# Kernel tuning notes

Measured on AMD Instinct MI355X. Metric: run time of the kernel, lower is better.

Reference implementation:

```python
import jax, jax.numpy as jnp
import numpy as np


def _edt_sq(binary):
    """Exact squared Euclidean distance transform of a 2D array.

    Nonzero pixels = foreground, zero pixels = background (scipy
    distance_transform_edt semantics). Computed as two separable 1D
    min-plus passes: d(i) = min_j (i-j)^2 + f(j), which is exact for EDT.
    """
    H, W = binary.shape
    INF = jnp.float32(H * H + W * W + 1)  # larger than any real sq distance
    f = jnp.where(binary == 0, jnp.float32(0.0), INF)  # [H, W]

    ih = jnp.arange(H, dtype=jnp.float32)
    sqh = (ih[:, None] - ih[None, :]) ** 2  # [H, H]
    # pass along rows (axis 0): d1[i, w] = min_j sqh[i, j] + f[j, w]
    d1 = jnp.min(sqh[:, :, None] + f[None, :, :], axis=1)  # [H, W]

    iw = jnp.arange(W, dtype=jnp.float32)
    sqw = (iw[:, None] - iw[None, :]) ** 2  # [W, W]
    # pass along cols (axis 1): d2[h, k] = min_l sqw[k, l] + d1[h, l]
    d2 = jnp.min(d1[:, None, :] + sqw[None, :, :], axis=2)  # [H, W]
    return d2


def setup_inputs() -> dict:
    key = jax.random.key(0)
    masks = jax.random.randint(key, (512, 512), 0, 2).astype(jnp.float32)
    return {"masks": masks}


def reference(masks):
    masks_n = masks / jnp.max(masks)          # masks / np.max(masks)
    dis_map = jnp.sqrt(_edt_sq(masks_n))      # distance_transform_edt
    skeleton = dis_map / jnp.max(dis_map)     # normalize
    boundary = masks_n - skeleton
    return (skeleton, boundary)
```

## Files before the change

kernel.cpp:

```cpp
#include <hip/hip_runtime.h>

#define H 512
#define W 512
#define N (H * W)
#define INF_SQ 524289.0f
#define KA_BLOCKS 1024
#define KB_BLOCKS 512

__global__ __launch_bounds__(256)
void edt2d_k(const float* __restrict__ masks, float* __restrict__ dis,
             float* __restrict__ pmaxm, float* __restrict__ pmaxd) {
    const int idx = blockIdx.x * 256 + threadIdx.x;
    const int y = idx >> 9, x = idx & (W - 1);

    const float v = masks[idx];
    float best = (v == 0.0f) ? 0.0f : INF_SQ;

    for (int r = 1; (float)(r * r) < best; ++r) {
        const int rr = r * r;
        const int ym = y - r, yp = y + r;
        const int x0 = max(x - r, 0), x1 = min(x + r, W - 1);
        if (ym >= 0) {
            const float* row = masks + ym * W;
            for (int x2 = x0; x2 <= x1; ++x2)
                if (row[x2] == 0.0f) {
                    const int dx = x2 - x;
                    best = fminf(best, (float)(dx * dx + rr));
                }
        }
        if (yp < H) {
            const float* row = masks + yp * W;
            for (int x2 = x0; x2 <= x1; ++x2)
                if (row[x2] == 0.0f) {
                    const int dx = x2 - x;
                    best = fminf(best, (float)(dx * dx + rr));
                }
        }
        const int y0 = max(y - r + 1, 0), y1 = min(y + r - 1, H - 1);
        if (x - r >= 0) {
            for (int y2 = y0; y2 <= y1; ++y2)
                if (masks[y2 * W + x - r] == 0.0f) {
                    const int dy = y2 - y;
                    best = fminf(best, (float)(dy * dy + rr));
                }
        }
        if (x + r < W) {
            for (int y2 = y0; y2 <= y1; ++y2)
                if (masks[y2 * W + x + r] == 0.0f) {
                    const int dy = y2 - y;
                    best = fminf(best, (float)(dy * dy + rr));
                }
        }
    }

    const float d = sqrtf(best);
    dis[idx] = d;

    float mm = v, md = d;
    for (int off = 32; off > 0; off >>= 1) {
        mm = fmaxf(mm, __shfl_down(mm, off, 64));
        md = fmaxf(md, __shfl_down(md, off, 64));
    }
    __shared__ float sm[4], sd[4];
    const int w = threadIdx.x >> 6, lane = threadIdx.x & 63;
    if (lane == 0) { sm[w] = mm; sd[w] = md; }
    __syncthreads();
    if (threadIdx.x == 0) {
        for (int i = 1; i < 4; ++i) { mm = fmaxf(mm, sm[i]); md = fmaxf(md, sd[i]); }
        pmaxm[blockIdx.x] = mm;
        pmaxd[blockIdx.x] = md;
    }
}

__global__ __launch_bounds__(128)
void finalize_k(const float* __restrict__ masks,
                const float* __restrict__ pmaxm,
                const float* __restrict__ pmaxd,
                float* __restrict__ out) {
    const int t = threadIdx.x;

    float mm = 0.0f, md = 0.0f;
#pragma unroll
    for (int i = 0; i < KA_BLOCKS / 128; ++i) {
        mm = fmaxf(mm, pmaxm[t + i * 128]);
        md = fmaxf(md, pmaxd[t + i * 128]);
    }
    for (int off = 32; off > 0; off >>= 1) {
        mm = fmaxf(mm, __shfl_down(mm, off, 64));
        md = fmaxf(md, __shfl_down(md, off, 64));
    }
    __shared__ float sm[2], sd[2];
    if ((t & 63) == 0) { sm[t >> 6] = mm; sd[t >> 6] = md; }
    __syncthreads();
    const float maxm = fmaxf(sm[0], sm[1]);
    const float maxd = fmaxf(sd[0], sd[1]);

    const int i = blockIdx.x * 128 + t;
    const float4 d4 = ((const float4*)out)[i];
    const float4 m4 = ((const float4*)masks)[i];
    float4 sk, bd;
    sk.x = d4.x / maxd; sk.y = d4.y / maxd; sk.z = d4.z / maxd; sk.w = d4.w / maxd;
    bd.x = m4.x / maxm - sk.x; bd.y = m4.y / maxm - sk.y;
    bd.z = m4.z / maxm - sk.z; bd.w = m4.w / maxm - sk.w;
    ((float4*)out)[i] = sk;
    ((float4*)out)[N / 4 + i] = bd;
}

extern "C" void kernel_launch(void* const* d_in, const int* in_sizes, int n_in,
                              void* d_out, int out_size, void* d_ws, size_t ws_size,
                              hipStream_t stream) {
    const float* masks = (const float*)d_in[0];
    float* out = (float*)d_out;
    float* pmaxm = (float*)d_ws;
    float* pmaxd = pmaxm + KA_BLOCKS;

    hipLaunchKernelGGL(edt2d_k, dim3(KA_BLOCKS), dim3(256), 0, stream, masks, out, pmaxm, pmaxd);
    hipLaunchKernelGGL(finalize_k, dim3(KB_BLOCKS), dim3(128), 0, stream, masks, pmaxm, pmaxd, out);
}
```

Baseline: 13.43 us.

## Process four pixels per thread with vectorized 3x3 neighborhood precheck

Each thread now handles four horizontally adjacent pixels, loading the three surrounding rows as float4 plus edge scalars and resolving the radius-1 ring from registers. Only pixels whose nearest background lies beyond distance one fall back to the ring-search loop, starting at radius 2. The EDT kernel's block count drops fourfold, and the finalize reduction reads fewer partial maxima. The change removes scattered scalar global loads for the common case but lowers thread-level parallelism and adds serialization when one of a thread's four pixels needs the slow path.

```diff
diff --git a/kernel.cpp b/kernel.cpp
--- a/kernel.cpp
+++ b/kernel.cpp
@@ -4,59 +4,105 @@
 #define W 512
 #define N (H * W)
 #define INF_SQ 524289.0f
-#define KA_BLOCKS 1024
+#define KA_BLOCKS 256
 #define KB_BLOCKS 512
 
 __global__ __launch_bounds__(256)
 void edt2d_k(const float* __restrict__ masks, float* __restrict__ dis,
              float* __restrict__ pmaxm, float* __restrict__ pmaxd) {
-    const int idx = blockIdx.x * 256 + threadIdx.x;
-    const int y = idx >> 9, x = idx & (W - 1);
+    const int tid = blockIdx.x * 256 + threadIdx.x;
+    const int y = tid >> 7;
+    const int q = tid & 127;
+    const int x0 = q << 2;
 
-    const float v = masks[idx];
-    float best = (v == 0.0f) ? 0.0f : INF_SQ;
+    const float4* m4 = (const float4*)masks;
+    const int yu = (y > 0) ? y - 1 : 0;
+    const int yd = (y < H - 1) ? y + 1 : H - 1;
 
-    for (int r = 1; (float)(r * r) < best; ++r) {
-        const int rr = r * r;
-        const int ym = y - r, yp = y + r;
-        const int x0 = max(x - r, 0), x1 = min(x + r, W - 1);
-        if (ym >= 0) {
-            const float* row = masks + ym * W;
-            for (int x2 = x0; x2 <= x1; ++x2)
-                if (row[x2] == 0.0f) {
-                    const int dx = x2 - x;
-                    best = fminf(best, (float)(dx * dx + rr));
-                }
-        }
-        if (yp < H) {
-            const float* row = masks + yp * W;
-            for (int x2 = x0; x2 <= x1; ++x2)
-                if (row[x2] == 0.0f) {
-                    const int dx = x2 - x;
-                    best = fminf(best, (float)(dx * dx + rr));
-                }
-        }
-        const int y0 = max(y - r + 1, 0), y1 = min(y + r - 1, H - 1);
-        if (x - r >= 0) {
-            for (int y2 = y0; y2 <= y1; ++y2)
-                if (masks[y2 * W + x - r] == 0.0f) {
-                    const int dy = y2 - y;
-                    best = fminf(best, (float)(dy * dy + rr));
-                }
-        }
-        if (x + r < W) {
-            for (int y2 = y0; y2 <= y1; ++y2)
-                if (masks[y2 * W + x + r] == 0.0f) {
-                    const int dy = y2 - y;
-                    best = fminf(best, (float)(dy * dy + rr));
-                }
-        }
+    const float4 u4 = m4[(yu << 7) + q];
+    const float4 c4 = m4[(y << 7) + q];
+    const float4 d4 = m4[(yd << 7) + q];
+
+    const int xl = (x0 > 0) ? x0 - 1 : 0;
+    const int xr = (x0 + 4 < W) ? x0 + 4 : W - 1;
+    const float ul = masks[yu * W + xl], ur = masks[yu * W + xr];
+    const float cl = masks[y * W + xl],  cr = masks[y * W + xr];
+    const float dl = masks[yd * W + xl], dr = masks[yd * W + xr];
+
+    const bool vy0 = (y > 0), vy1 = (y < H - 1);
+    const bool vx0 = (x0 > 0), vx1 = (x0 + 4 < W);
+
+    const float rowU[6] = {ul, u4.x, u4.y, u4.z, u4.w, ur};
+    const float rowC[6] = {cl, c4.x, c4.y, c4.z, c4.w, cr};
+    const float rowD[6] = {dl, d4.x, d4.y, d4.z, d4.w, dr};
+
+    float best[4];
+#pragma unroll
+    for (int j = 0; j < 4; ++j) {
+        const bool lv = (j > 0) || vx0;
+        const bool rv = (j < 3) || vx1;
+        float b = INF_SQ;
+        b = fminf(b, (vy0 && lv && rowU[j] == 0.0f)     ? 2.0f : INF_SQ);
+        b = fminf(b, (vy0 &&       rowU[j + 1] == 0.0f) ? 1.0f : INF_SQ);
+        b = fminf(b, (vy0 && rv && rowU[j + 2] == 0.0f) ? 2.0f : INF_SQ);
+        b = fminf(b, (lv &&        rowC[j] == 0.0f)     ? 1.0f : INF_SQ);
+        b = fminf(b, (rv &&        rowC[j + 2] == 0.0f) ? 1.0f : INF_SQ);
+        b = fminf(b, (vy1 && lv && rowD[j] == 0.0f)     ? 2.0f : INF_SQ);
+        b = fminf(b, (vy1 &&       rowD[j + 1] == 0.0f) ? 1.0f : INF_SQ);
+        b = fminf(b, (vy1 && rv && rowD[j + 2] == 0.0f) ? 2.0f : INF_SQ);
+        best[j] = (rowC[j + 1] == 0.0f) ? 0.0f : b;
     }
 
-    const float d = sqrtf(best);
-    dis[idx] = d;
+#pragma unroll
+    for (int j = 0; j < 4; ++j) {
+        const int x = x0 + j;
+        float b = best[j];
+        for (int r = 2; (float)(r * r) < b; ++r) {
+            const int rr = r * r;
+            const int ymr = y - r, ypr = y + r;
+            const int xa = max(x - r, 0), xb = min(x + r, W - 1);
+            if (ymr >= 0) {
+                const float* row = masks + ymr * W;
+                for (int x2 = xa; x2 <= xb; ++x2)
+                    if (row[x2] == 0.0f) {
+                        const int dx = x2 - x;
+                        b = fminf(b, (float)(dx * dx + rr));
+                    }
+            }
+            if (ypr < H) {
+                const float* row = masks + ypr * W;
+                for (int x2 = xa; x2 <= xb; ++x2)
+                    if (row[x2] == 0.0f) {
+                        const int dx = x2 - x;
+                        b = fminf(b, (float)(dx * dx + rr));
+                    }
+            }
+            const int y0 = max(y - r + 1, 0), y1 = min(y + r - 1, H - 1);
+            if (x - r >= 0) {
+                for (int y2 = y0; y2 <= y1; ++y2)
+                    if (masks[y2 * W + x - r] == 0.0f) {
+                        const int dy = y2 - y;
+                        b = fminf(b, (float)(dy * dy + rr));
+                    }
+            }
+            if (x + r < W) {
+                for (int y2 = y0; y2 <= y1; ++y2)
+                    if (masks[y2 * W + x + r] == 0.0f) {
+                        const int dy = y2 - y;
+                        b = fminf(b, (float)(dy * dy + rr));
+                    }
+            }
+        }
+        best[j] = b;
+    }
 
-    float mm = v, md = d;
+    float4 o;
+    o.x = sqrtf(best[0]); o.y = sqrtf(best[1]);
+    o.z = sqrtf(best[2]); o.w = sqrtf(best[3]);
+    ((float4*)dis)[tid] = o;
+
+    float mm = fmaxf(fmaxf(c4.x, c4.y), fmaxf(c4.z, c4.w));
+    float md = fmaxf(fmaxf(o.x, o.y), fmaxf(o.z, o.w));
     for (int off = 32; off > 0; off >>= 1) {
         mm = fmaxf(mm, __shfl_down(mm, off, 64));
         md = fmaxf(md, __shfl_down(md, off, 64));
@@ -79,12 +125,8 @@
                 float* __restrict__ out) {
     const int t = threadIdx.x;
 
-    float mm = 0.0f, md = 0.0f;
-#pragma unroll
-    for (int i = 0; i < KA_BLOCKS / 128; ++i) {
-        mm = fmaxf(mm, pmaxm[t + i * 128]);
-        md = fmaxf(md, pmaxd[t + i * 128]);
-    }
+    float mm = fmaxf(pmaxm[t], pmaxm[t + 128]);
+    float md = fmaxf(pmaxd[t], pmaxd[t + 128]);
     for (int off = 32; off > 0; off >>= 1) {
         mm = fmaxf(mm, __shfl_down(mm, off, 64));
         md = fmaxf(md, __shfl_down(md, off, 64));
@@ -96,10 +138,10 @@
     const float maxd = fmaxf(sd[0], sd[1]);
 
     const int i = blockIdx.x * 128 + t;
-    const float4 d4 = ((const float4*)out)[i];
+    const float4 dd = ((const float4*)out)[i];
     const float4 m4 = ((const float4*)masks)[i];
     float4 sk, bd;
-    sk.x = d4.x / maxd; sk.y = d4.y / maxd; sk.z = d4.z / maxd; sk.w = d4.w / maxd;
+    sk.x = dd.x / maxd; sk.y = dd.y / maxd; sk.z = dd.z / maxd; sk.w = dd.w / maxd;
     bd.x = m4.x / maxm - sk.x; bd.y = m4.y / maxm - sk.y;
     bd.z = m4.z / maxm - sk.z; bd.w = m4.w / maxm - sk.w;
     ((float4*)out)[i] = sk;
```

Result: slower. 17.82 us (+32.7%).
